# Optimization experiments

Measured on AMD Instinct MI355X. Metric: run time of the kernel, lower is better.

The kernel has to match this reference:

```python
import jax, jax.numpy as jnp
import numpy as np

NUM_SEQS = 8
SEQ_LEN = 2048
HIDDEN = 768
NUM_HEADS = 12
HEAD_DIM = 64
EPS = 1e-12


def setup_inputs() -> dict:
    key = jax.random.key(0)
    ks = jax.random.split(key, 12)
    total = NUM_SEQS * SEQ_LEN
    hidden_states = jax.random.normal(ks[0], (total, HIDDEN), dtype=jnp.float32)
    cu_seq_lens = jnp.arange(NUM_SEQS + 1, dtype=jnp.int32) * SEQ_LEN
    s = 0.02
    inp = {
        "hidden_states": hidden_states,
        "cu_seq_lens": cu_seq_lens,
        "max_seq_len": SEQ_LEN,
        "norm_w": jnp.ones((HIDDEN,), jnp.float32),
        "norm_b": jnp.zeros((HIDDEN,), jnp.float32),
        "Wq": jax.random.normal(ks[1], (HIDDEN, HIDDEN), jnp.float32) * s,
        "bq": jnp.zeros((HIDDEN,), jnp.float32),
        "Wk": jax.random.normal(ks[2], (HIDDEN, HIDDEN), jnp.float32) * s,
        "bk": jnp.zeros((HIDDEN,), jnp.float32),
        "Wv": jax.random.normal(ks[3], (HIDDEN, HIDDEN), jnp.float32) * s,
        "bv": jnp.zeros((HIDDEN,), jnp.float32),
        "Wo": jax.random.normal(ks[4], (HIDDEN, HIDDEN), jnp.float32) * s,
        "bo": jnp.zeros((HIDDEN,), jnp.float32),
    }
    return inp


def _layer_norm(x, w, b):
    mu = jnp.mean(x, axis=-1, keepdims=True)
    var = jnp.mean(jnp.square(x - mu), axis=-1, keepdims=True)
    return (x - mu) * jax.lax.rsqrt(var + EPS) * w + b


def _rope(x, positions, interleaved=False):
    # x: [t, h, d]; positions: [t]
    d = x.shape[-1]
    inv_freq = 1.0 / (10000.0 ** (jnp.arange(0, d, 2, dtype=jnp.float32) / d))  # [d/2]
    theta = positions.astype(jnp.float32)[:, None] * inv_freq[None, :]  # [t, d/2]
    cos = jnp.cos(theta)[:, None, :]  # [t, 1, d/2]
    sin = jnp.sin(theta)[:, None, :]
    x1, x2 = x[..., : d // 2], x[..., d // 2 :]
    return jnp.concatenate([x1 * cos - x2 * sin, x2 * cos + x1 * sin], axis=-1)


def _attention(q, k, v):
    # q,k,v: [b, s, h, d] (equal-length sequences, no padding)
    scale = 1.0 / jnp.sqrt(jnp.asarray(q.shape[-1], q.dtype))
    scores = jnp.einsum("bqhd,bkhd->bhqk", q, k) * scale
    probs = jax.nn.softmax(scores, axis=-1)
    return jnp.einsum("bhqk,bkhd->bqhd", probs, v)


def reference(hidden_states, cu_seq_lens, max_seq_len, norm_w, norm_b,
              Wq, bq, Wk, bk, Wv, bv, Wo, bo):
    t = hidden_states.shape[0]
    # pre_norm, layer_idx=1 -> LayerNorm
    x = _layer_norm(hidden_states, norm_w, norm_b)
    value = x @ Wv + bv
    query = x @ Wq + bq
    key = x @ Wk + bk

    def split(z):
        return z.reshape(t, NUM_HEADS, HEAD_DIM)

    q, k, v = split(query), split(key), split(value)

    # positions within each sequence (equal-length packing)
    positions = jnp.tile(jnp.arange(SEQ_LEN, dtype=jnp.int32), NUM_SEQS)
    q = _rope(q, positions)
    k = _rope(k, positions)

    # reshape packed -> [b, s, h, d]; sequences are equal-length here
    qb = q.reshape(NUM_SEQS, SEQ_LEN, NUM_HEADS, HEAD_DIM)
    kb = k.reshape(NUM_SEQS, SEQ_LEN, NUM_HEADS, HEAD_DIM)
    vb = v.reshape(NUM_SEQS, SEQ_LEN, NUM_HEADS, HEAD_DIM)
    attn = _attention(qb, kb, vb).reshape(t, HIDDEN)

    attn = attn @ Wo + bo
    # residual add (dropout prob = 0)
    out = attn + x
    return out
```

## Files before the change

### kernel.cpp

```cpp
#include <hip/hip_runtime.h>

typedef __bf16 bf16x8 __attribute__((ext_vector_type(8)));
typedef float  f32x4  __attribute__((ext_vector_type(4)));
typedef float  f32x16 __attribute__((ext_vector_type(16)));
typedef unsigned u32x2 __attribute__((ext_vector_type(2)));

#define MFMA16(a,b,c) __builtin_amdgcn_mfma_f32_16x16x32_bf16((a),(b),(c),0,0,0)
#define MFMA32(a,b,c) __builtin_amdgcn_mfma_f32_32x32x16_bf16((a),(b),(c),0,0,0)

constexpr int  HID  = 768;
constexpr long T    = 16384;
constexpr long SZ   = T * HID;
constexpr int  SEQ  = 2048;
constexpr int  NH   = 12;
constexpr int  HD   = 64;
constexpr int  WELE = HID * HID;

constexpr float QSCALE = 0.125f * 1.4426950408889634f;
constexpr float L10K32 = 13.287712379549449f / 32.0f;

__device__ __forceinline__ unsigned pkbf(float a, float b) {
    union { __bf16 h[2]; unsigned u; } x;
    x.h[0] = (__bf16)a; x.h[1] = (__bf16)b; return x.u;
}

__device__ __forceinline__ void gld16(const __bf16* g, __bf16* l) {
    __builtin_amdgcn_global_load_lds(
        (const __attribute__((address_space(1))) unsigned int*)g,
        (__attribute__((address_space(3))) unsigned int*)l, 16, 0, 0);
}

__global__ __launch_bounds__(256)
void wconv_kernel(const float* __restrict__ W0, __bf16* __restrict__ T0,
                  const float* __restrict__ W1, __bf16* __restrict__ T1,
                  const float* __restrict__ W2, __bf16* __restrict__ T2,
                  const float* __restrict__ W3, __bf16* __restrict__ T3) {
    const float* W; __bf16* Wt;
    switch (blockIdx.z) {
        case 0: W = W0; Wt = T0; break;
        case 1: W = W1; Wt = T1; break;
        case 2: W = W2; Wt = T2; break;
        default: W = W3; Wt = T3; break;
    }
    __shared__ float tile[64][65];
    int n0 = blockIdx.x * 64, k0 = blockIdx.y * 64;
    int c = threadIdx.x & 63, rr = threadIdx.x >> 6;
#pragma unroll
    for (int i = 0; i < 16; i++) {
        int r = i * 4 + rr;
        tile[r][c] = W[(long)(k0 + r) * HID + n0 + c];
    }
    __syncthreads();
#pragma unroll
    for (int i = 0; i < 16; i++) {
        int r = i * 4 + rr;
        Wt[(long)(n0 + r) * HID + k0 + c] = (__bf16)tile[c][r];
    }
}

__global__ __launch_bounds__(256)
void ln_kernel(const float* __restrict__ hs, const float* __restrict__ w,
               const float* __restrict__ b, __bf16* __restrict__ xbf) {
    int row = blockIdx.x, tid = threadIdx.x;
    const float* hr = hs + (long)row * HID;
    float v0 = hr[tid], v1 = hr[tid + 256], v2 = hr[tid + 512];
    float s  = v0 + v1 + v2;
    float s2 = v0 * v0 + v1 * v1 + v2 * v2;
#pragma unroll
    for (int off = 1; off < 64; off <<= 1) {
        s  += __shfl_xor(s, off);
        s2 += __shfl_xor(s2, off);
    }
    __shared__ float red[8];
    int wave = tid >> 6;
    if ((tid & 63) == 0) { red[wave] = s; red[4 + wave] = s2; }
    __syncthreads();
    s  = red[0] + red[1] + red[2] + red[3];
    s2 = red[4] + red[5] + red[6] + red[7];
    float mu   = s * (1.0f / HID);
    float var  = s2 * (1.0f / HID) - mu * mu;
    float rstd = rsqrtf(var + 1e-12f);
    long base = (long)row * HID;
    xbf[base + tid]       = (__bf16)((v0 - mu) * rstd * w[tid]       + b[tid]);
    xbf[base + tid + 256] = (__bf16)((v1 - mu) * rstd * w[tid + 256] + b[tid + 256]);
    xbf[base + tid + 512] = (__bf16)((v2 - mu) * rstd * w[tid + 512] + b[tid + 512]);
}

constexpr int SEGSZ = 528;

template <int MODE>
__global__ __launch_bounds__(256)
void gemm_lds(const __bf16* __restrict__ A, const __bf16* __restrict__ Bt,
              const float* __restrict__ bias, __bf16* __restrict__ outb,
              const __bf16* __restrict__ resid, float* __restrict__ outf,
              float scale) {
    int tid = threadIdx.x, wave = tid >> 6, lane = tid & 63;
    int lr = lane & 15, quad = lane >> 4;
    int wm = wave >> 1, wn = wave & 1;
    long m0 = (long)blockIdx.x * 128;
    int  n0 = blockIdx.y * 128;

    __shared__ __align__(16) __bf16 As[16 * SEGSZ];
    __shared__ __align__(16) __bf16 Bs[16 * SEGSZ];

    const f32x4 vzero = {0.f, 0.f, 0.f, 0.f};
    f32x4 acc[4][4];
#pragma unroll
    for (int ms = 0; ms < 4; ms++)
#pragma unroll
        for (int ns = 0; ns < 4; ns++) acc[ms][ns] = vzero;

    const __bf16* ga = A  + (long)(m0 + wave * 32 + (lane >> 3)) * HID + (lane & 7) * 8;
    const __bf16* gb = Bt + (long)(n0 + wave * 32 + (lane >> 3)) * HID + (lane & 7) * 8;
    __bf16* la = As + wave * 4 * SEGSZ;
    __bf16* lb = Bs + wave * 4 * SEGSZ;

    int fbase = (lr >> 3) * SEGSZ + (lr & 7) * 64 + quad * 8;

    for (int k0 = 0; k0 < HID; k0 += 64) {
#pragma unroll
        for (int j = 0; j < 4; j++) {
            gld16(ga + (long)j * 8 * HID + k0, la + j * SEGSZ);
            gld16(gb + (long)j * 8 * HID + k0, lb + j * SEGSZ);
        }
        __syncthreads();
#pragma unroll
        for (int kk = 0; kk < 64; kk += 32) {
            bf16x8 af[4], bfr[4];
#pragma unroll
            for (int ms = 0; ms < 4; ms++)
                af[ms] = *(const bf16x8*)&As[fbase + (wm * 8 + ms * 2) * SEGSZ + kk];
#pragma unroll
            for (int ns = 0; ns < 4; ns++)
                bfr[ns] = *(const bf16x8*)&Bs[fbase + (wn * 8 + ns * 2) * SEGSZ + kk];
#pragma unroll
            for (int ms = 0; ms < 4; ms++)
#pragma unroll
                for (int ns = 0; ns < 4; ns++)
                    acc[ms][ns] = MFMA16(af[ms], bfr[ns], acc[ms][ns]);
        }
        __syncthreads();
    }

    if (MODE == 1) {
#pragma unroll
        for (int ms = 0; ms < 4; ms++)
#pragma unroll
        for (int r = 0; r < 4; r++) {
            int d = (int)(m0 + wm * 64 + ms * 16 + quad * 4 + r);
            float bv = bias[d];
            int hh = d >> 6, dd = d & 63;
#pragma unroll
            for (int ns = 0; ns < 4; ns++) {
                int posg = n0 + wn * 64 + ns * 16 + lr;
                int sq = posg >> 11, pos = posg & (SEQ - 1);
                outb[((long)((sq * NH + hh) * HD + dd) << 11) + pos] =
                    (__bf16)(acc[ms][ns][r] + bv);
            }
        }
    } else {
#pragma unroll
        for (int ns = 0; ns < 4; ns++) {
            int col = n0 + wn * 64 + ns * 16 + lr;
            float bv = bias[col];
#pragma unroll
            for (int ms = 0; ms < 4; ms++)
#pragma unroll
            for (int r = 0; r < 4; r++) {
                long row = m0 + wm * 64 + ms * 16 + quad * 4 + r;
                outf[row * HID + col] = acc[ms][ns][r] + bv + (float)resid[row * HID + col];
            }
        }
    }
}

__global__ __launch_bounds__(256, 2)
void gemm_qk(const __bf16* __restrict__ A, const __bf16* __restrict__ Btq,
             const __bf16* __restrict__ Btk,
             const float* __restrict__ biasq, const float* __restrict__ biask,
             __bf16* __restrict__ outq, __bf16* __restrict__ outk) {
    int tid = threadIdx.x, wave = tid >> 6, lane = tid & 63;
    int lr = lane & 15, quad = lane >> 4;
    int wm = wave >> 1, wn = wave & 1;
    long m0 = (long)blockIdx.x * 128;
    int  n0 = blockIdx.y * 128;

    __shared__ __align__(16) __bf16 As[16 * SEGSZ];
    __shared__ __align__(16) __bf16 Bqs[16 * SEGSZ];
    __shared__ __align__(16) __bf16 Bks[16 * SEGSZ];

    const f32x4 vzero = {0.f, 0.f, 0.f, 0.f};
    f32x4 accq[4][4], acck[4][4];
#pragma unroll
    for (int ms = 0; ms < 4; ms++)
#pragma unroll
        for (int ns = 0; ns < 4; ns++) { accq[ms][ns] = vzero; acck[ms][ns] = vzero; }

    const __bf16* ga = A   + (long)(m0 + wave * 32 + (lane >> 3)) * HID + (lane & 7) * 8;
    const __bf16* gq = Btq + (long)(n0 + wave * 32 + (lane >> 3)) * HID + (lane & 7) * 8;
    const __bf16* gk = Btk + (long)(n0 + wave * 32 + (lane >> 3)) * HID + (lane & 7) * 8;
    __bf16* la = As  + wave * 4 * SEGSZ;
    __bf16* lq = Bqs + wave * 4 * SEGSZ;
    __bf16* lk = Bks + wave * 4 * SEGSZ;

    int fbase = (lr >> 3) * SEGSZ + (lr & 7) * 64 + quad * 8;

    for (int k0 = 0; k0 < HID; k0 += 64) {
#pragma unroll
        for (int j = 0; j < 4; j++) {
            gld16(ga + (long)j * 8 * HID + k0, la + j * SEGSZ);
            gld16(gq + (long)j * 8 * HID + k0, lq + j * SEGSZ);
            gld16(gk + (long)j * 8 * HID + k0, lk + j * SEGSZ);
        }
        __syncthreads();
#pragma unroll
        for (int kk = 0; kk < 64; kk += 32) {
            bf16x8 af[4], bqf[4], bkf[4];
#pragma unroll
            for (int ms = 0; ms < 4; ms++)
                af[ms] = *(const bf16x8*)&As[fbase + (wm * 8 + ms * 2) * SEGSZ + kk];
#pragma unroll
            for (int ns = 0; ns < 4; ns++) {
                bqf[ns] = *(const bf16x8*)&Bqs[fbase + (wn * 8 + ns * 2) * SEGSZ + kk];
                bkf[ns] = *(const bf16x8*)&Bks[fbase + (wn * 8 + ns * 2) * SEGSZ + kk];
            }
#pragma unroll
            for (int ms = 0; ms < 4; ms++)
#pragma unroll
                for (int ns = 0; ns < 4; ns++) {
                    accq[ms][ns] = MFMA16(af[ms], bqf[ns], accq[ms][ns]);
                    acck[ms][ns] = MFMA16(af[ms], bkf[ns], acck[ms][ns]);
                }
        }
        __syncthreads();
    }

    int hb = n0 + wn * 64;
    float f1 = __builtin_amdgcn_exp2f(-(float)lr * L10K32);
    float f2 = __builtin_amdgcn_exp2f(-(float)(lr + 16) * L10K32);
    {
        float b0 = biasq[hb + lr],      b1 = biasq[hb + 16 + lr];
        float b2 = biasq[hb + 32 + lr], b3 = biasq[hb + 48 + lr];
#pragma unroll
        for (int ms = 0; ms < 4; ms++)
#pragma unroll
        for (int r = 0; r < 4; r++) {
            long row = m0 + wm * 64 + ms * 16 + quad * 4 + r;
            int pos = (int)(row & (SEQ - 1));
            float s1, c1, s2, c2;
            __sincosf((float)pos * f1, &s1, &c1);
            __sincosf((float)pos * f2, &s2, &c2);
            float v0 = accq[ms][0][r] + b0, v1 = accq[ms][1][r] + b1;
            float v2 = accq[ms][2][r] + b2, v3 = accq[ms][3][r] + b3;
            __bf16* ob = outq + row * HID + hb;
            ob[lr]      = (__bf16)((v0 * c1 - v2 * s1) * QSCALE);
            ob[16 + lr] = (__bf16)((v1 * c2 - v3 * s2) * QSCALE);
            ob[32 + lr] = (__bf16)((v2 * c1 + v0 * s1) * QSCALE);
            ob[48 + lr] = (__bf16)((v3 * c2 + v1 * s2) * QSCALE);
        }
    }
    {
        float b0 = biask[hb + lr],      b1 = biask[hb + 16 + lr];
        float b2 = biask[hb + 32 + lr], b3 = biask[hb + 48 + lr];
#pragma unroll
        for (int ms = 0; ms < 4; ms++)
#pragma unroll
        for (int r = 0; r < 4; r++) {
            long row = m0 + wm * 64 + ms * 16 + quad * 4 + r;
            int pos = (int)(row & (SEQ - 1));
            float s1, c1, s2, c2;
            __sincosf((float)pos * f1, &s1, &c1);
            __sincosf((float)pos * f2, &s2, &c2);
            float v0 = acck[ms][0][r] + b0, v1 = acck[ms][1][r] + b1;
            float v2 = acck[ms][2][r] + b2, v3 = acck[ms][3][r] + b3;
            __bf16* ob = outk + row * HID + hb;
            ob[lr]      = (__bf16)(v0 * c1 - v2 * s1);
            ob[16 + lr] = (__bf16)(v1 * c2 - v3 * s2);
            ob[32 + lr] = (__bf16)(v2 * c1 + v0 * s1);
            ob[48 + lr] = (__bf16)(v3 * c2 + v1 * s2);
        }
    }
}

__global__ __launch_bounds__(512)
void attn_kernel(const __bf16* __restrict__ q, const __bf16* __restrict__ k,
                 const __bf16* __restrict__ vt, __bf16* __restrict__ att) {
    int tid = threadIdx.x, wave = tid >> 6, lane = tid & 63;
    int c = lane & 31, hi = lane >> 5;
    int bb = blockIdx.x;
    int s  = bb & 7;
    int ii = bb >> 3;
    int h  = ii >> 3;
    int qt = ii & 7;
    long q0 = (long)s * SEQ + qt * 256 + wave * 32;

    __shared__ __align__(16) __bf16 KV[6 * 4096];

    bf16x8 qf[4];
    {
        const __bf16* qrow = q + (q0 + c) * HID + h * HD + hi * 8;
#pragma unroll
        for (int kk = 0; kk < 4; kk++)
            qf[kk] = *(const bf16x8*)(qrow + kk * 16);
    }

    f32x16 o[2] = {};
    float ls = 0.f;

    const __bf16* kg = k  + (long)s * SEQ * HID + h * HD;
    const __bf16* vg = vt + (long)(s * NH + h) * HD * SEQ;

    int srow = lane >> 3;
    int sgch = (lane & 7) ^ srow;

    const __bf16* pb4[4];
#pragma unroll
    for (int kk = 0; kk < 4; kk++)
        pb4[kk] = KV + c * 64 + ((((kk << 1) + hi) ^ (c & 7)) << 3);

#define STAGE(bufi, kv)                                                         \
    {                                                                           \
        gld16(kg + (long)((kv) + wave * 8 + srow) * HID + sgch * 8,             \
              KV + (bufi) * 4096 + wave * 512);                                 \
        gld16(vg + (long)(wave * 8 + srow) * SEQ + (kv) + sgch * 8,             \
              KV + 12288 + (bufi) * 4096 + wave * 512);                         \
    }

#define ATTN_BODY(BUF)                                                          \
    {                                                                           \
        f32x16 st0 = {}, st1 = {};                                              \
        __builtin_amdgcn_s_setprio(1);                                          \
        _Pragma("unroll")                                                       \
        for (int kk = 0; kk < 4; kk++) {                                        \
            bf16x8 kf0 = *(const bf16x8*)(pb4[kk] + (BUF) * 4096);              \
            st0 = MFMA32(kf0, qf[kk], st0);                                     \
            bf16x8 kf1 = *(const bf16x8*)(pb4[kk] + (BUF) * 4096 + 2048);       \
            st1 = MFMA32(kf1, qf[kk], st1);                                     \
        }                                                                       \
        __builtin_amdgcn_s_setprio(0);                                          \
        bf16x8 pb[4];                                                           \
        _Pragma("unroll")                                                       \
        for (int kh = 0; kh < 2; kh++) {                                        \
            unsigned pk[8];                                                     \
            _Pragma("unroll")                                                   \
            for (int i = 0; i < 8; i++) {                                       \
                float e0 = __builtin_amdgcn_exp2f(kh ? st1[2 * i] : st0[2 * i]);        \
                float e1 = __builtin_amdgcn_exp2f(kh ? st1[2 * i + 1] : st0[2 * i + 1]);\
                ls += e0 + e1;                                                  \
                pk[i] = pkbf(e0, e1);                                           \
            }                                                                   \
            _Pragma("unroll")                                                   \
            for (int b = 0; b < 2; b++) {                                       \
                u32x2 r02 = __builtin_amdgcn_permlane32_swap(                   \
                    pk[4 * b + 0], pk[4 * b + 2], false, false);                \
                u32x2 r13 = __builtin_amdgcn_permlane32_swap(                   \
                    pk[4 * b + 1], pk[4 * b + 3], false, false);                \
                union { unsigned u[4]; bf16x8 v; } pu;                          \
                pu.u[0] = r02[0]; pu.u[1] = r13[0];                             \
                pu.u[2] = r02[1]; pu.u[3] = r13[1];                             \
                pb[2 * kh + b] = pu.v;                                          \
            }                                                                   \
        }                                                                       \
        __builtin_amdgcn_s_setprio(1);                                          \
        _Pragma("unroll")                                                       \
        for (int kk = 0; kk < 4; kk++) {                                        \
            bf16x8 vf0 = *(const bf16x8*)(pb4[kk] + 12288 + (BUF) * 4096);      \
            o[0] = MFMA32(vf0, pb[kk], o[0]);                                   \
            bf16x8 vf1 = *(const bf16x8*)(pb4[kk] + 12288 + (BUF) * 4096 + 2048); \
            o[1] = MFMA32(vf1, pb[kk], o[1]);                                   \
        }                                                                       \
        __builtin_amdgcn_s_setprio(0);                                          \
    }

#define WAITV(N) asm volatile("s_waitcnt vmcnt(" #N ")" ::: "memory")
#define BAR()    asm volatile("s_barrier" ::: "memory")

    STAGE(0, 0)
    STAGE(1, 64)

#pragma unroll 1
    for (int u = 0; u < 10; u++) {
        int kv = u * 3 * 64;
        WAITV(2); BAR();
        STAGE(2, kv + 2 * 64)
        ATTN_BODY(0)
        WAITV(2); BAR();
        STAGE(0, kv + 3 * 64)
        ATTN_BODY(1)
        WAITV(2); BAR();
        STAGE(1, kv + 4 * 64)
        ATTN_BODY(2)
    }
    WAITV(2); BAR();
    ATTN_BODY(0)
    WAITV(0); BAR();
    ATTN_BODY(1)

#undef WAITV
#undef BAR
#undef STAGE
#undef ATTN_BODY

    ls += __shfl_xor(ls, 32);
    float inv = 1.0f / ls;
    __bf16* ob = att + (q0 + c) * HID + h * HD;
#pragma unroll
    for (int dh = 0; dh < 2; dh++)
#pragma unroll
        for (int a = 0; a < 4; a++) {
            unsigned lo  = pkbf(o[dh][4 * a] * inv,     o[dh][4 * a + 1] * inv);
            unsigned hi2 = pkbf(o[dh][4 * a + 2] * inv, o[dh][4 * a + 3] * inv);
            int d = dh * 32 + a * 8 + hi * 4;
            *(unsigned long long*)&ob[d] =
                ((unsigned long long)hi2 << 32) | lo;
        }
}

extern "C" void kernel_launch(void* const* d_in, const int* in_sizes, int n_in,
                              void* d_out, int out_size, void* d_ws, size_t ws_size,
                              hipStream_t stream) {
    const float* hs    = (const float*)d_in[0];
    const float* normw = (const float*)d_in[3];
    const float* normb = (const float*)d_in[4];
    const float* Wq = (const float*)d_in[5];
    const float* bq = (const float*)d_in[6];
    const float* Wk = (const float*)d_in[7];
    const float* bk = (const float*)d_in[8];
    const float* Wv = (const float*)d_in[9];
    const float* bv = (const float*)d_in[10];
    const float* Wo = (const float*)d_in[11];
    const float* bo = (const float*)d_in[12];

    __bf16* base = (__bf16*)d_ws;
    __bf16* x   = base;
    __bf16* qb  = base + SZ;
    __bf16* kb  = base + 2 * SZ;
    __bf16* vtb = base + 3 * SZ;
    __bf16* att = base + 4 * SZ;
    __bf16* wqt = base + 5 * SZ;
    __bf16* wkt = wqt + WELE;
    __bf16* wvt = wkt + WELE;
    __bf16* wot = wvt + WELE;

    wconv_kernel<<<dim3(12, 12, 4), 256, 0, stream>>>(Wq, wqt, Wk, wkt, Wv, wvt, Wo, wot);

    ln_kernel<<<(int)T, 256, 0, stream>>>(hs, normw, normb, x);

    gemm_qk<<<dim3(T / 128, HID / 128), 256, 0, stream>>>(x, wqt, wkt, bq, bk, qb, kb);
    gemm_lds<1><<<dim3(HID / 128, T / 128), 256, 0, stream>>>(wvt, x, bv, vtb, nullptr, nullptr, 1.0f);

    attn_kernel<<<dim3(NH * 8 * 8), 512, 0, stream>>>(qb, kb, vtb, att);

    gemm_lds<2><<<dim3(T / 128, HID / 128), 256, 0, stream>>>(att, wot, bo, nullptr, x, (float*)d_out, 1.0f);
}
```

Baseline: 387.4 us.

## Double-buffer LDS tiles in projection GEMMs to overlap loads with MFMA

Converts the generic gemm_lds and the fused Q/K gemm_qk from a load-sync-compute-sync loop to a software-pipelined loop, using raw s_waitcnt vmcnt and s_barrier instead of __syncthreads. gemm_lds double-buffers both A and B tiles; gemm_qk double-buffers only A and reloads the Q/K weight tiles into a single buffer between compute phases. The goal is to hide global-to-LDS latency behind MFMA work. In exchange, LDS use grows, which may reduce occupancy, and the hand-counted vmcnt values must exactly match the number of outstanding loads.

```diff
diff --git a/kernel.cpp b/kernel.cpp
--- a/kernel.cpp
+++ b/kernel.cpp
@@ -29,6 +29,9 @@
         (const __attribute__((address_space(1))) unsigned int*)g,
         (__attribute__((address_space(3))) unsigned int*)l, 16, 0, 0);
 }
+
+#define WAITVN(N) asm volatile("s_waitcnt vmcnt(" #N ")" ::: "memory")
+#define BARR()    asm volatile("s_barrier" ::: "memory")
 
 __global__ __launch_bounds__(256)
 void wconv_kernel(const float* __restrict__ W0, __bf16* __restrict__ T0,
@@ -87,6 +90,7 @@
 }
 
 constexpr int SEGSZ = 528;
+constexpr int BUFSZ = 16 * SEGSZ;
 
 template <int MODE>
 __global__ __launch_bounds__(256)
@@ -100,8 +104,8 @@
     long m0 = (long)blockIdx.x * 128;
     int  n0 = blockIdx.y * 128;
 
-    __shared__ __align__(16) __bf16 As[16 * SEGSZ];
-    __shared__ __align__(16) __bf16 Bs[16 * SEGSZ];
+    __shared__ __align__(16) __bf16 As[2][BUFSZ];
+    __shared__ __align__(16) __bf16 Bs[2][BUFSZ];
 
     const f32x4 vzero = {0.f, 0.f, 0.f, 0.f};
     f32x4 acc[4][4];
@@ -112,35 +116,49 @@
 
     const __bf16* ga = A  + (long)(m0 + wave * 32 + (lane >> 3)) * HID + (lane & 7) * 8;
     const __bf16* gb = Bt + (long)(n0 + wave * 32 + (lane >> 3)) * HID + (lane & 7) * 8;
-    __bf16* la = As + wave * 4 * SEGSZ;
-    __bf16* lb = Bs + wave * 4 * SEGSZ;
 
     int fbase = (lr >> 3) * SEGSZ + (lr & 7) * 64 + quad * 8;
 
-    for (int k0 = 0; k0 < HID; k0 += 64) {
-#pragma unroll
-        for (int j = 0; j < 4; j++) {
-            gld16(ga + (long)j * 8 * HID + k0, la + j * SEGSZ);
-            gld16(gb + (long)j * 8 * HID + k0, lb + j * SEGSZ);
-        }
-        __syncthreads();
-#pragma unroll
-        for (int kk = 0; kk < 64; kk += 32) {
-            bf16x8 af[4], bfr[4];
-#pragma unroll
-            for (int ms = 0; ms < 4; ms++)
-                af[ms] = *(const bf16x8*)&As[fbase + (wm * 8 + ms * 2) * SEGSZ + kk];
-#pragma unroll
-            for (int ns = 0; ns < 4; ns++)
-                bfr[ns] = *(const bf16x8*)&Bs[fbase + (wn * 8 + ns * 2) * SEGSZ + kk];
-#pragma unroll
-            for (int ms = 0; ms < 4; ms++)
-#pragma unroll
-                for (int ns = 0; ns < 4; ns++)
-                    acc[ms][ns] = MFMA16(af[ms], bfr[ns], acc[ms][ns]);
-        }
-        __syncthreads();
-    }
+#define GSTAGE(b, k0)                                                           \
+    {                                                                           \
+        _Pragma("unroll")                                                       \
+        for (int j = 0; j < 4; j++) {                                           \
+            gld16(ga + (long)j * 8 * HID + (k0), As[b] + wave * 4 * SEGSZ + j * SEGSZ); \
+            gld16(gb + (long)j * 8 * HID + (k0), Bs[b] + wave * 4 * SEGSZ + j * SEGSZ); \
+        }                                                                       \
+    }
+
+#define GCOMP(b)                                                                \
+    {                                                                           \
+        _Pragma("unroll")                                                       \
+        for (int kk = 0; kk < 64; kk += 32) {                                   \
+            bf16x8 af[4], bfr[4];                                               \
+            _Pragma("unroll")                                                   \
+            for (int ms = 0; ms < 4; ms++)                                      \
+                af[ms] = *(const bf16x8*)&As[b][fbase + (wm * 8 + ms * 2) * SEGSZ + kk]; \
+            _Pragma("unroll")                                                   \
+            for (int ns = 0; ns < 4; ns++)                                      \
+                bfr[ns] = *(const bf16x8*)&Bs[b][fbase + (wn * 8 + ns * 2) * SEGSZ + kk]; \
+            _Pragma("unroll")                                                   \
+            for (int ms = 0; ms < 4; ms++)                                      \
+                _Pragma("unroll")                                               \
+                for (int ns = 0; ns < 4; ns++)                                  \
+                    acc[ms][ns] = MFMA16(af[ms], bfr[ns], acc[ms][ns]);         \
+        }                                                                       \
+    }
+
+    GSTAGE(0, 0)
+#pragma unroll 1
+    for (int u = 0; u < 5; u++) {
+        int k0 = u * 128;
+        GSTAGE(1, k0 + 64)  WAITVN(8); BARR(); GCOMP(0) BARR();
+        GSTAGE(0, k0 + 128) WAITVN(8); BARR(); GCOMP(1) BARR();
+    }
+    GSTAGE(1, 11 * 64) WAITVN(8); BARR(); GCOMP(0) BARR();
+    WAITVN(0); BARR(); GCOMP(1)
+
+#undef GSTAGE
+#undef GCOMP
 
     if (MODE == 1) {
 #pragma unroll
@@ -185,9 +203,9 @@
     long m0 = (long)blockIdx.x * 128;
     int  n0 = blockIdx.y * 128;
 
-    __shared__ __align__(16) __bf16 As[16 * SEGSZ];
-    __shared__ __align__(16) __bf16 Bqs[16 * SEGSZ];
-    __shared__ __align__(16) __bf16 Bks[16 * SEGSZ];
+    __shared__ __align__(16) __bf16 As[2][BUFSZ];
+    __shared__ __align__(16) __bf16 Bqs[BUFSZ];
+    __shared__ __align__(16) __bf16 Bks[BUFSZ];
 
     const f32x4 vzero = {0.f, 0.f, 0.f, 0.f};
     f32x4 accq[4][4], acck[4][4];
@@ -199,41 +217,64 @@
     const __bf16* ga = A   + (long)(m0 + wave * 32 + (lane >> 3)) * HID + (lane & 7) * 8;
     const __bf16* gq = Btq + (long)(n0 + wave * 32 + (lane >> 3)) * HID + (lane & 7) * 8;
     const __bf16* gk = Btk + (long)(n0 + wave * 32 + (lane >> 3)) * HID + (lane & 7) * 8;
-    __bf16* la = As  + wave * 4 * SEGSZ;
-    __bf16* lq = Bqs + wave * 4 * SEGSZ;
-    __bf16* lk = Bks + wave * 4 * SEGSZ;
 
     int fbase = (lr >> 3) * SEGSZ + (lr & 7) * 64 + quad * 8;
 
-    for (int k0 = 0; k0 < HID; k0 += 64) {
-#pragma unroll
-        for (int j = 0; j < 4; j++) {
-            gld16(ga + (long)j * 8 * HID + k0, la + j * SEGSZ);
-            gld16(gq + (long)j * 8 * HID + k0, lq + j * SEGSZ);
-            gld16(gk + (long)j * 8 * HID + k0, lk + j * SEGSZ);
-        }
-        __syncthreads();
-#pragma unroll
-        for (int kk = 0; kk < 64; kk += 32) {
-            bf16x8 af[4], bqf[4], bkf[4];
-#pragma unroll
-            for (int ms = 0; ms < 4; ms++)
-                af[ms] = *(const bf16x8*)&As[fbase + (wm * 8 + ms * 2) * SEGSZ + kk];
-#pragma unroll
-            for (int ns = 0; ns < 4; ns++) {
-                bqf[ns] = *(const bf16x8*)&Bqs[fbase + (wn * 8 + ns * 2) * SEGSZ + kk];
-                bkf[ns] = *(const bf16x8*)&Bks[fbase + (wn * 8 + ns * 2) * SEGSZ + kk];
-            }
-#pragma unroll
-            for (int ms = 0; ms < 4; ms++)
-#pragma unroll
-                for (int ns = 0; ns < 4; ns++) {
-                    accq[ms][ns] = MFMA16(af[ms], bqf[ns], accq[ms][ns]);
-                    acck[ms][ns] = MFMA16(af[ms], bkf[ns], acck[ms][ns]);
-                }
-        }
-        __syncthreads();
-    }
+#define QSTAGE_A(b, k0)                                                         \
+    {                                                                           \
+        _Pragma("unroll")                                                       \
+        for (int j = 0; j < 4; j++)                                             \
+            gld16(ga + (long)j * 8 * HID + (k0), As[b] + wave * 4 * SEGSZ + j * SEGSZ); \
+    }
+#define QSTAGE_B(k0)                                                            \
+    {                                                                           \
+        _Pragma("unroll")                                                       \
+        for (int j = 0; j < 4; j++) {                                           \
+            gld16(gq + (long)j * 8 * HID + (k0), Bqs + wave * 4 * SEGSZ + j * SEGSZ); \
+            gld16(gk + (long)j * 8 * HID + (k0), Bks + wave * 4 * SEGSZ + j * SEGSZ); \
+        }                                                                       \
+    }
+#define QCOMP(b)                                                                \
+    {                                                                           \
+        _Pragma("unroll")                                                       \
+        for (int kk = 0; kk < 64; kk += 32) {                                   \
+            bf16x8 af[4], bqf[4], bkf[4];                                       \
+            _Pragma("unroll")                                                   \
+            for (int ms = 0; ms < 4; ms++)                                      \
+                af[ms] = *(const bf16x8*)&As[b][fbase + (wm * 8 + ms * 2) * SEGSZ + kk]; \
+            _Pragma("unroll")                                                   \
+            for (int ns = 0; ns < 4; ns++) {                                    \
+                bqf[ns] = *(const bf16x8*)&Bqs[fbase + (wn * 8 + ns * 2) * SEGSZ + kk]; \
+                bkf[ns] = *(const bf16x8*)&Bks[fbase + (wn * 8 + ns * 2) * SEGSZ + kk]; \
+            }                                                                   \
+            _Pragma("unroll")                                                   \
+            for (int ms = 0; ms < 4; ms++)                                      \
+                _Pragma("unroll")                                               \
+                for (int ns = 0; ns < 4; ns++) {                                \
+                    accq[ms][ns] = MFMA16(af[ms], bqf[ns], accq[ms][ns]);       \
+                    acck[ms][ns] = MFMA16(af[ms], bkf[ns], acck[ms][ns]);       \
+                }                                                               \
+        }                                                                       \
+    }
+
+    QSTAGE_A(0, 0) QSTAGE_B(0) QSTAGE_A(1, 64)
+    WAITVN(4); BARR();
+
+#pragma unroll 1
+    for (int u = 0; u < 5; u++) {
+        int k0 = u * 128;
+        QCOMP(0) BARR();
+        QSTAGE_B(k0 + 64)  QSTAGE_A(0, k0 + 128) WAITVN(4); BARR();
+        QCOMP(1) BARR();
+        QSTAGE_B(k0 + 128) QSTAGE_A(1, k0 + 192) WAITVN(4); BARR();
+    }
+    QCOMP(0) BARR();
+    QSTAGE_B(11 * 64) WAITVN(0); BARR();
+    QCOMP(1)
+
+#undef QSTAGE_A
+#undef QSTAGE_B
+#undef QCOMP
 
     int hb = n0 + wn * 64;
     float f1 = __builtin_amdgcn_exp2f(-(float)lr * L10K32);
@@ -372,32 +413,27 @@
         __builtin_amdgcn_s_setprio(0);                                          \
     }
 
-#define WAITV(N) asm volatile("s_waitcnt vmcnt(" #N ")" ::: "memory")
-#define BAR()    asm volatile("s_barrier" ::: "memory")
-
     STAGE(0, 0)
     STAGE(1, 64)
 
 #pragma unroll 1
     for (int u = 0; u < 10; u++) {
         int kv = u * 3 * 64;
-        WAITV(2); BAR();
+        WAITVN(2); BARR();
         STAGE(2, kv + 2 * 64)
         ATTN_BODY(0)
-        WAITV(2); BAR();
+        WAITVN(2); BARR();
         STAGE(0, kv + 3 * 64)
         ATTN_BODY(1)
-        WAITV(2); BAR();
+        WAITVN(2); BARR();
         STAGE(1, kv + 4 * 64)
         ATTN_BODY(2)
     }
-    WAITV(2); BAR();
+    WAITVN(2); BARR();
     ATTN_BODY(0)
-    WAITV(0); BAR();
+    WAITVN(0); BARR();
     ATTN_BODY(1)
 
-#undef WAITV
-#undef BAR
 #undef STAGE
 #undef ATTN_BODY
 
```

After: 380.7 us. About the same (-1.7%).
